# Optimization experiments

Hardware: AMD Instinct MI355X
Metric: run time of the kernel (lower is better)

## Reference

```python
import jax, jax.numpy as jnp
import numpy as np

B, T, D = 32, 4096, 512  # D = 2 * hidden_size


def setup_inputs() -> dict:
    key = jax.random.key(0)
    k_h, k_w1, k_b1, k_w2 = jax.random.split(key, 4)
    scale = 1.0 / np.sqrt(D)
    return {
        "hidden_states": jax.random.normal(k_h, (B, T, D), dtype=jnp.float32),
        "W1": jax.random.normal(k_w1, (D, D), dtype=jnp.float32) * scale,
        "b1": jax.random.normal(k_b1, (D,), dtype=jnp.float32) * scale,
        "W2": jax.random.normal(k_w2, (D, D), dtype=jnp.float32) * scale,
    }


def reference(hidden_states, W1, b1, W2):
    # u = tanh(h @ W1^T + b1)        [B, T, D]
    u = jnp.tanh(jnp.einsum("btd,ed->bte", hidden_states, W1) + b1)
    # alphas = softmax over time axis of u @ W2^T (no bias)   [B, T, D]
    alphas = jax.nn.softmax(jnp.einsum("btd,ed->bte", u, W2), axis=1)
    # Original loop cats weighted [T, D] slices along dim 0 then sums dim 0,
    # i.e. a global reduction over batch AND time -> [D]
    return jnp.sum(hidden_states * alphas, axis=(0, 1))
```

## Files before the change

kernel.cpp:

```cpp
#include <hip/hip_runtime.h>
#include <hip/hip_bf16.h>
#include <math.h>

#define BATCH 32
#define TLEN  4096
#define DDIM  512
#define BM    64
#define BLOCK 1024

typedef __attribute__((ext_vector_type(8))) short bf16x8;
typedef __attribute__((ext_vector_type(4))) float f32x4;
typedef __attribute__((ext_vector_type(4))) short s16x4;

__device__ __forceinline__ short f32_to_bf16_rne(float f) {
    union { float f; unsigned int u; } v; v.f = f;
    unsigned int r = (v.u + 0x7FFFu + ((v.u >> 16) & 1u)) >> 16;
    return (short)r;
}
__device__ __forceinline__ float fast_tanh(float x) {
    x = fminf(fmaxf(x, -15.f), 15.f);
    float t = __expf(2.0f * x);
    return (t - 1.0f) / (t + 1.0f);
}

__device__ __forceinline__ int lds_idx(int r, int c) {
    int g = (c >> 3) ^ (r & 31);
    return r * DDIM + (g << 3) + (c & 7);
}

__global__ void prep_kernel(const float* __restrict__ W1, const float* __restrict__ W2,
                            short* __restrict__ W1b, short* __restrict__ W2b,
                            float* __restrict__ lbuf, float* __restrict__ gbuf) {
    int i = blockIdx.x * blockDim.x + threadIdx.x;
    W1b[i] = f32_to_bf16_rne(W1[i]);
    W2b[i] = f32_to_bf16_rne(W2[i]);
    if (i < BATCH * DDIM) { lbuf[i] = 0.f; gbuf[i] = 0.f; }
}

__global__ __launch_bounds__(BLOCK, 4)
void main_kernel(const float* __restrict__ h,
                 const short* __restrict__ W1b,
                 const float* __restrict__ b1,
                 const short* __restrict__ W2b,
                 float* __restrict__ lbuf, float* __restrict__ gbuf) {
    __shared__ short sh[BM * DDIM];

    const int tid  = threadIdx.x;
    const int row0 = blockIdx.x * BM;
    const int b    = row0 / TLEN;

    {
        const float4* hp = (const float4*)(h + (size_t)row0 * DDIM);
        #pragma unroll
        for (int i = 0; i < (BM * DDIM / 4) / BLOCK; ++i) {
            int idx  = tid + i * BLOCK;
            float4 v = hp[idx];
            int flat = idx * 4;
            int r = flat >> 9;
            int c = flat & (DDIM - 1);
            s16x4 p;
            p.x = f32_to_bf16_rne(v.x); p.y = f32_to_bf16_rne(v.y);
            p.z = f32_to_bf16_rne(v.z); p.w = f32_to_bf16_rne(v.w);
            *(s16x4*)&sh[lds_idx(r, c)] = p;
        }
    }
    __syncthreads();

    const int wave  = tid >> 6;
    const int lane  = tid & 63;
    const int quad  = lane >> 4;
    const int l16   = lane & 15;
    const int wcol0 = wave * 32;
    const int kq    = quad * 8;

    f32x4 acc[4][2];
    #pragma unroll
    for (int rb = 0; rb < 4; ++rb)
        #pragma unroll
        for (int cb = 0; cb < 2; ++cb) acc[rb][cb] = (f32x4){0.f, 0.f, 0.f, 0.f};

    {
        const short* Bb = W1b + (size_t)(wcol0 + l16) * DDIM + kq;
        bf16x8 bcur[2], bnxt[2];
        #pragma unroll
        for (int cb = 0; cb < 2; ++cb)
            bcur[cb] = *(const bf16x8*)(Bb + cb * 16 * DDIM);

        for (int k0 = 0; k0 < DDIM; k0 += 32) {
            bf16x8 af[4];
            #pragma unroll
            for (int rb = 0; rb < 4; ++rb)
                af[rb] = *(const bf16x8*)&sh[lds_idx(rb * 16 + l16, k0 + kq)];
            #pragma unroll
            for (int cb = 0; cb < 2; ++cb)
                bnxt[cb] = *(const bf16x8*)(Bb + cb * 16 * DDIM + k0 + 32);
            #pragma unroll
            for (int cb = 0; cb < 2; ++cb)
                #pragma unroll
                for (int rb = 0; rb < 4; ++rb)
                    acc[rb][cb] = __builtin_amdgcn_mfma_f32_16x16x32_bf16(
                        af[rb], bcur[cb], acc[rb][cb], 0, 0, 0);
            #pragma unroll
            for (int cb = 0; cb < 2; ++cb) bcur[cb] = bnxt[cb];
        }
    }

    __syncthreads();

    #pragma unroll
    for (int cb = 0; cb < 2; ++cb) {
        int col  = wcol0 + cb * 16 + l16;
        float bias = b1[col];
        #pragma unroll
        for (int rb = 0; rb < 4; ++rb)
            #pragma unroll
            for (int r = 0; r < 4; ++r) {
                int row = rb * 16 + quad * 4 + r;
                sh[lds_idx(row, col)] =
                    f32_to_bf16_rne(fast_tanh(acc[rb][cb][r] + bias));
            }
    }
    __syncthreads();

    #pragma unroll
    for (int rb = 0; rb < 4; ++rb)
        #pragma unroll
        for (int cb = 0; cb < 2; ++cb) acc[rb][cb] = (f32x4){0.f, 0.f, 0.f, 0.f};

    {
        const short* Bb = W2b + (size_t)(wcol0 + l16) * DDIM + kq;
        bf16x8 bcur[2], bnxt[2];
        #pragma unroll
        for (int cb = 0; cb < 2; ++cb)
            bcur[cb] = *(const bf16x8*)(Bb + cb * 16 * DDIM);

        for (int k0 = 0; k0 < DDIM; k0 += 32) {
            bf16x8 af[4];
            #pragma unroll
            for (int rb = 0; rb < 4; ++rb)
                af[rb] = *(const bf16x8*)&sh[lds_idx(rb * 16 + l16, k0 + kq)];
            #pragma unroll
            for (int cb = 0; cb < 2; ++cb)
                bnxt[cb] = *(const bf16x8*)(Bb + cb * 16 * DDIM + k0 + 32);
            #pragma unroll
            for (int cb = 0; cb < 2; ++cb)
                #pragma unroll
                for (int rb = 0; rb < 4; ++rb)
                    acc[rb][cb] = __builtin_amdgcn_mfma_f32_16x16x32_bf16(
                        af[rb], bcur[cb], acc[rb][cb], 0, 0, 0);
            #pragma unroll
            for (int cb = 0; cb < 2; ++cb) bcur[cb] = bnxt[cb];
        }
    }

    #pragma unroll
    for (int cb = 0; cb < 2; ++cb) {
        int col = wcol0 + cb * 16 + l16;
        float hv[16];
        #pragma unroll
        for (int rb = 0; rb < 4; ++rb)
            #pragma unroll
            for (int r = 0; r < 4; ++r)
                hv[rb * 4 + r] =
                    h[(size_t)(row0 + rb * 16 + quad * 4 + r) * DDIM + col];
        float lsum = 0.f, gsum = 0.f;
        #pragma unroll
        for (int rb = 0; rb < 4; ++rb)
            #pragma unroll
            for (int r = 0; r < 4; ++r) {
                float e = __expf(acc[rb][cb][r]);
                lsum += e;
                gsum += e * hv[rb * 4 + r];
            }
        lsum += __shfl_xor(lsum, 16);  lsum += __shfl_xor(lsum, 32);
        gsum += __shfl_xor(gsum, 16);  gsum += __shfl_xor(gsum, 32);
        if (quad == 0) {
            atomicAdd(&lbuf[b * DDIM + col], lsum);
            atomicAdd(&gbuf[b * DDIM + col], gsum);
        }
    }
}

__global__ void finish_kernel(const float* __restrict__ lbuf,
                              const float* __restrict__ gbuf,
                              float* __restrict__ out) {
    int d = blockIdx.x * blockDim.x + threadIdx.x;
    float s = 0.f;
    #pragma unroll
    for (int b = 0; b < BATCH; ++b)
        s += gbuf[b * DDIM + d] / lbuf[b * DDIM + d];
    out[d] = s;
}

extern "C" void kernel_launch(void* const* d_in, const int* in_sizes, int n_in,
                              void* d_out, int out_size, void* d_ws, size_t ws_size,
                              hipStream_t stream) {
    const float* h  = (const float*)d_in[0];
    const float* W1 = (const float*)d_in[1];
    const float* b1 = (const float*)d_in[2];
    const float* W2 = (const float*)d_in[3];
    float* out = (float*)d_out;

    char* ws = (char*)d_ws;
    short* W1b = (short*)ws;
    short* W2b = (short*)(ws + 512 * 1024);
    float* lbuf = (float*)(ws + 1024 * 1024);
    float* gbuf = (float*)(ws + 1024 * 1024 + 64 * 1024);

    prep_kernel<<<(DDIM * DDIM) / 256, 256, 0, stream>>>(W1, W2, W1b, W2b, lbuf, gbuf);
    main_kernel<<<(BATCH * TLEN) / BM, BLOCK, 0, stream>>>(h, W1b, b1, W2b, lbuf, gbuf);
    finish_kernel<<<2, 256, 0, stream>>>(lbuf, gbuf, out);
}
```

Measured before the change: 641.7 us.

## Halve block to 512 threads with each wave covering two column passes

The block shrinks from 16 to 8 waves, and each wave now computes two 32-column slices in sequential passes for both GEMMs. The first pass's tanh outputs are packed into registers as bf16 pairs and written to LDS after the second pass, and the second GEMM's softmax epilogue runs per pass. The aim is to change the work split and occupancy (launch bounds move to 512 threads with 2 blocks per CU) and to cut per-block sync cost, at the price of more registers per thread and longer serial work per wave.

```diff
diff --git a/kernel.cpp b/kernel.cpp
--- a/kernel.cpp
+++ b/kernel.cpp
@@ -6,7 +6,7 @@
 #define TLEN  4096
 #define DDIM  512
 #define BM    64
-#define BLOCK 1024
+#define BLOCK 512
 
 typedef __attribute__((ext_vector_type(8))) short bf16x8;
 typedef __attribute__((ext_vector_type(4))) float f32x4;
@@ -16,6 +16,11 @@
     union { float f; unsigned int u; } v; v.f = f;
     unsigned int r = (v.u + 0x7FFFu + ((v.u >> 16) & 1u)) >> 16;
     return (short)r;
+}
+__device__ __forceinline__ float bf16_to_f32(short s) {
+    union { unsigned int u; float f; } v;
+    v.u = ((unsigned int)(unsigned short)s) << 16;
+    return v.f;
 }
 __device__ __forceinline__ float fast_tanh(float x) {
     x = fminf(fmaxf(x, -15.f), 15.f);
@@ -37,7 +42,7 @@
     if (i < BATCH * DDIM) { lbuf[i] = 0.f; gbuf[i] = 0.f; }
 }
 
-__global__ __launch_bounds__(BLOCK, 4)
+__global__ __launch_bounds__(BLOCK, 2)
 void main_kernel(const float* __restrict__ h,
                  const short* __restrict__ W1b,
                  const float* __restrict__ b1,
@@ -66,21 +71,24 @@
     }
     __syncthreads();
 
-    const int wave  = tid >> 6;
-    const int lane  = tid & 63;
-    const int quad  = lane >> 4;
-    const int l16   = lane & 15;
-    const int wcol0 = wave * 32;
-    const int kq    = quad * 8;
-
+    const int wave = tid >> 6;
+    const int lane = tid & 63;
+    const int quad = lane >> 4;
+    const int l16  = lane & 15;
+    const int kq   = quad * 8;
+
+    unsigned int u0pk[16];
     f32x4 acc[4][2];
-    #pragma unroll
-    for (int rb = 0; rb < 4; ++rb)
-        #pragma unroll
-        for (int cb = 0; cb < 2; ++cb) acc[rb][cb] = (f32x4){0.f, 0.f, 0.f, 0.f};
-
-    {
-        const short* Bb = W1b + (size_t)(wcol0 + l16) * DDIM + kq;
+
+    #pragma unroll
+    for (int pass = 0; pass < 2; ++pass) {
+        const int col0 = wave * 32 + pass * 256;
+        #pragma unroll
+        for (int rb = 0; rb < 4; ++rb)
+            #pragma unroll
+            for (int cb = 0; cb < 2; ++cb) acc[rb][cb] = (f32x4){0.f,0.f,0.f,0.f};
+
+        const short* Bb = W1b + (size_t)(col0 + l16) * DDIM + kq;
         bf16x8 bcur[2], bnxt[2];
         #pragma unroll
         for (int cb = 0; cb < 2; ++cb)
@@ -103,32 +111,53 @@
             #pragma unroll
             for (int cb = 0; cb < 2; ++cb) bcur[cb] = bnxt[cb];
         }
+
+        #pragma unroll
+        for (int cb = 0; cb < 2; ++cb) {
+            float bias = b1[col0 + cb * 16 + l16];
+            #pragma unroll
+            for (int rb = 0; rb < 4; ++rb)
+                #pragma unroll
+                for (int r = 0; r < 4; ++r)
+                    acc[rb][cb][r] = fast_tanh(acc[rb][cb][r] + bias);
+        }
+        if (pass == 0) {
+            #pragma unroll
+            for (int rb = 0; rb < 4; ++rb)
+                #pragma unroll
+                for (int r = 0; r < 4; ++r)
+                    u0pk[rb * 4 + r] =
+                        ((unsigned int)(unsigned short)f32_to_bf16_rne(acc[rb][0][r])) |
+                        (((unsigned int)(unsigned short)f32_to_bf16_rne(acc[rb][1][r])) << 16);
+        }
     }
 
     __syncthreads();
 
     #pragma unroll
     for (int cb = 0; cb < 2; ++cb) {
-        int col  = wcol0 + cb * 16 + l16;
-        float bias = b1[col];
+        int c0 = wave * 32 + cb * 16 + l16;
+        int c1 = c0 + 256;
         #pragma unroll
         for (int rb = 0; rb < 4; ++rb)
             #pragma unroll
             for (int r = 0; r < 4; ++r) {
                 int row = rb * 16 + quad * 4 + r;
-                sh[lds_idx(row, col)] =
-                    f32_to_bf16_rne(fast_tanh(acc[rb][cb][r] + bias));
+                sh[lds_idx(row, c0)] = (short)(u0pk[rb * 4 + r] >> (cb * 16));
+                sh[lds_idx(row, c1)] = f32_to_bf16_rne(acc[rb][cb][r]);
             }
     }
     __syncthreads();
 
     #pragma unroll
-    for (int rb = 0; rb < 4; ++rb)
-        #pragma unroll
-        for (int cb = 0; cb < 2; ++cb) acc[rb][cb] = (f32x4){0.f, 0.f, 0.f, 0.f};
-
-    {
-        const short* Bb = W2b + (size_t)(wcol0 + l16) * DDIM + kq;
+    for (int pass = 0; pass < 2; ++pass) {
+        const int col0 = wave * 32 + pass * 256;
+        #pragma unroll
+        for (int rb = 0; rb < 4; ++rb)
+            #pragma unroll
+            for (int cb = 0; cb < 2; ++cb) acc[rb][cb] = (f32x4){0.f,0.f,0.f,0.f};
+
+        const short* Bb = W2b + (size_t)(col0 + l16) * DDIM + kq;
         bf16x8 bcur[2], bnxt[2];
         #pragma unroll
         for (int cb = 0; cb < 2; ++cb)
@@ -151,32 +180,32 @@
             #pragma unroll
             for (int cb = 0; cb < 2; ++cb) bcur[cb] = bnxt[cb];
         }
-    }
-
-    #pragma unroll
-    for (int cb = 0; cb < 2; ++cb) {
-        int col = wcol0 + cb * 16 + l16;
-        float hv[16];
-        #pragma unroll
-        for (int rb = 0; rb < 4; ++rb)
-            #pragma unroll
-            for (int r = 0; r < 4; ++r)
-                hv[rb * 4 + r] =
-                    h[(size_t)(row0 + rb * 16 + quad * 4 + r) * DDIM + col];
-        float lsum = 0.f, gsum = 0.f;
-        #pragma unroll
-        for (int rb = 0; rb < 4; ++rb)
-            #pragma unroll
-            for (int r = 0; r < 4; ++r) {
-                float e = __expf(acc[rb][cb][r]);
-                lsum += e;
-                gsum += e * hv[rb * 4 + r];
+
+        #pragma unroll
+        for (int cb = 0; cb < 2; ++cb) {
+            int col = col0 + cb * 16 + l16;
+            float hv[16];
+            #pragma unroll
+            for (int rb = 0; rb < 4; ++rb)
+                #pragma unroll
+                for (int r = 0; r < 4; ++r)
+                    hv[rb * 4 + r] =
+                        h[(size_t)(row0 + rb * 16 + quad * 4 + r) * DDIM + col];
+            float lsum = 0.f, gsum = 0.f;
+            #pragma unroll
+            for (int rb = 0; rb < 4; ++rb)
+                #pragma unroll
+                for (int r = 0; r < 4; ++r) {
+                    float e = __expf(acc[rb][cb][r]);
+                    lsum += e;
+                    gsum += e * hv[rb * 4 + r];
+                }
+            lsum += __shfl_xor(lsum, 16);  lsum += __shfl_xor(lsum, 32);
+            gsum += __shfl_xor(gsum, 16);  gsum += __shfl_xor(gsum, 32);
+            if (quad == 0) {
+                atomicAdd(&lbuf[b * DDIM + col], lsum);
+                atomicAdd(&gbuf[b * DDIM + col], gsum);
             }
-        lsum += __shfl_xor(lsum, 16);  lsum += __shfl_xor(lsum, 32);
-        gsum += __shfl_xor(gsum, 16);  gsum += __shfl_xor(gsum, 32);
-        if (quad == 0) {
-            atomicAdd(&lbuf[b * DDIM + col], lsum);
-            atomicAdd(&gbuf[b * DDIM + col], gsum);
         }
     }
 }
```

Result: no change. 641.7 us (-0.0%).
